# Kernel optimization log

Hardware: AMD Instinct MI355X
Metric: run time of the kernel (lower is better)

Reference implementation:

```python
import jax, jax.numpy as jnp
import numpy as np

K_SIZE, STRIDE, PAD = 3, 1, 1
B, C1, C2, H, W = 2, 256, 256, 64, 64


def conv2d(x, w, b, stride, pad):
    out = jax.lax.conv_general_dilated(
        x, w, (stride, stride), [(pad, pad), (pad, pad)],
        dimension_numbers=("NCHW", "OIHW", "NCHW"))
    return out + b[None, :, None, None]


def deform_conv2d(x, offset, mask, w, b, k, stride, pad):
    # torchvision.ops.deform_conv2d semantics (modulated, offset_groups=1)
    Bn, C, Hh, Ww = x.shape
    Ho, Wo = offset.shape[2], offset.shape[3]
    K = k * k
    # offset channels are (dy, dx) interleaved per kernel point
    off = offset.reshape(Bn, K, 2, Ho, Wo)
    dy, dx = off[:, :, 0], off[:, :, 1]          # [B,K,Ho,Wo]
    ki = jnp.arange(k)
    kyy, kxx = jnp.meshgrid(ki, ki, indexing="ij")
    kyy, kxx = kyy.reshape(K), kxx.reshape(K)
    base_y = (jnp.arange(Ho) * stride - pad)[None, :, None] + kyy[:, None, None]  # [K,Ho,1]
    base_x = (jnp.arange(Wo) * stride - pad)[None, None, :] + kxx[:, None, None]  # [K,1,Wo]
    ys = base_y[None].astype(x.dtype) + dy       # [B,K,Ho,Wo]
    xs = base_x[None].astype(x.dtype) + dx
    N = K * Ho * Wo
    ysf, xsf = ys.reshape(Bn, N), xs.reshape(Bn, N)
    y0 = jnp.floor(ysf)
    x0 = jnp.floor(xsf)
    ly, lx = ysf - y0, xsf - x0                  # bilinear fractions
    y0i, x0i = y0.astype(jnp.int32), x0.astype(jnp.int32)
    xf = x.reshape(Bn, C, Hh * Ww)

    def gather(yi, xi):
        valid = (yi >= 0) & (yi < Hh) & (xi >= 0) & (xi < Ww)
        idx = jnp.clip(yi, 0, Hh - 1) * Ww + jnp.clip(xi, 0, Ww - 1)
        v = jnp.take_along_axis(xf, idx[:, None, :], axis=2)  # [B,C,N]
        return v * valid[:, None, :].astype(x.dtype)

    v00 = gather(y0i, x0i)
    v01 = gather(y0i, x0i + 1)
    v10 = gather(y0i + 1, x0i)
    v11 = gather(y0i + 1, x0i + 1)
    wy1, wx1 = ly[:, None], lx[:, None]
    val = (v00 * (1 - wy1) * (1 - wx1) + v01 * (1 - wy1) * wx1 +
           v10 * wy1 * (1 - wx1) + v11 * wy1 * wx1)          # [B,C,N]
    val = val.reshape(Bn, C, K, Ho, Wo) * mask[:, None]       # modulate
    out = jnp.einsum("ock,bckhw->bohw", w.reshape(w.shape[0], C, K), val)
    return out + b[None, :, None, None]


def setup_inputs() -> dict:
    key = jax.random.key(0)
    ks = jax.random.split(key, 6)
    k2 = K_SIZE * K_SIZE
    return {
        "x": jax.random.normal(ks[0], (B, C1, H, W), jnp.float32),
        "offset_feat": jax.random.normal(ks[1], (B, C2, H, W), jnp.float32),
        # offset/mask head conv (zero-init in module; small random so offsets are non-trivial)
        "w_offset_mask": jax.random.normal(ks[2], (3 * k2, C2, K_SIZE, K_SIZE), jnp.float32) * 0.01,
        "b_offset_mask": jax.random.normal(ks[3], (3 * k2,), jnp.float32) * 0.01,
        "w_dcn": jax.random.normal(ks[4], (C2, C1, K_SIZE, K_SIZE), jnp.float32) / np.sqrt(C1 * k2),
        "b_dcn": jax.random.normal(ks[5], (C2,), jnp.float32) * 0.01,
    }


def reference(x, offset_feat, w_offset_mask, b_offset_mask, w_dcn, b_dcn):
    om = conv2d(offset_feat, w_offset_mask, b_offset_mask, STRIDE, PAD)  # [B,3*k*k,Ho,Wo]
    o1, o2, m = jnp.split(om, 3, axis=1)
    offset = jnp.concatenate([o1, o2], axis=1)   # [B,2*k*k,Ho,Wo]
    mask = jax.nn.sigmoid(m)                      # [B,k*k,Ho,Wo]
    return deform_conv2d(x, offset, mask, w_dcn, b_dcn, K_SIZE, STRIDE, PAD)
```

## Files before the change

### kernel.cpp

```cpp
#include <hip/hip_runtime.h>
#include <math.h>

#define BATCH 2
#define CIN   256
#define COUT  256
#define HWPIX 4096
#define CKTOT 2304
#define VSTR  40
#define PH    66
#define PHW   4356
#define VBUF  (288 * VSTR)

typedef __attribute__((ext_vector_type(8))) short short8;
typedef __attribute__((ext_vector_type(2))) float float2v;
typedef __attribute__((ext_vector_type(4))) float float4v;

__device__ __forceinline__ unsigned short f2bf(float f) {
    unsigned u = __float_as_uint(f);
    unsigned r = (u + 0x7FFFu + ((u >> 16) & 1u)) >> 16;
    return (unsigned short)r;
}
__device__ __forceinline__ float bf2f(unsigned short h) {
    return __uint_as_float(((unsigned)h) << 16);
}
__device__ __forceinline__ unsigned cvtpk_bf16(float a, float b) {
    unsigned r;
    asm("v_cvt_pk_bf16_f32 %0, %1, %2" : "=v"(r) : "v"(a), "v"(b));
    return r;
}
__device__ __forceinline__ float2v unpk(unsigned u) {
    float2v r;
    r.x = __uint_as_float(u << 16);
    r.y = __uint_as_float(u & 0xffff0000u);
    return r;
}

__global__ __launch_bounds__(256) void prep_kernel(
    const float* __restrict__ x, const float* __restrict__ feat,
    const float* __restrict__ wdcn, const float* __restrict__ wom,
    unsigned short* __restrict__ xTh,
    unsigned short* __restrict__ fh,
    unsigned short* __restrict__ whi,
    unsigned short* __restrict__ wohi)
{
    const int bid = blockIdx.x;
    const int tid = threadIdx.x;

    if (bid < 4096) {
        const bool isx = bid < 2048;
        const int lb = isx ? bid : bid - 2048;
        const int b  = lb >> 10;
        const int r  = lb & 1023;
        const int pt = r >> 3;
        const int ct = r & 7;
        __shared__ float t[32][33];
        const int tx = tid & 31, ty = tid >> 5;
        const float* src = isx ? x : feat;
        const float* sb = src + ((size_t)b * 256 + ct * 32) * HWPIX + pt * 32;
#pragma unroll
        for (int i = ty; i < 32; i += 8)
            t[i][tx] = sb[(size_t)i * HWPIX + tx];
        __syncthreads();
        const int px = tid >> 3;
        const int c4 = (tid & 7) << 2;
        float a0 = t[c4][px], a1 = t[c4 + 1][px];
        float a2 = t[c4 + 2][px], a3 = t[c4 + 3][px];
        uint2 rv = make_uint2(cvtpk_bf16(a0, a1), cvtpk_bf16(a2, a3));
        if (isx) {
            *(uint2*)&xTh[((size_t)b * HWPIX + pt * 32 + px) * 256 + ct * 32 + c4] = rv;
        } else {
            int p = pt * 32 + px;
            int row = (p >> 6) + 1, col = (p & 63) + 1;
            *(uint2*)&fh[((size_t)b * PHW + row * PH + col) * 256 + ct * 32 + c4] = rv;
        }
    } else if (bid < 5248) {
        int g2 = (bid - 4096) * 256 + tid;
        int e  = g2 * 2;
        int cc  = e & 31;
        int co  = (e >> 5) & 255;
        int kcb = e >> 13;
        int k   = kcb >> 3;
        int cb  = kcb & 7;
        const float* s = wdcn + ((size_t)co * 256 + cb * 32 + cc) * 9 + k;
        *(unsigned*)&whi[e] = cvtpk_bf16(s[0], s[9]);
    } else if (bid < 5536) {
        int gid = (bid - 5248) * 256 + tid;
        int cc  = gid & 31;
        int co  = (gid >> 5) & 31;
        int kcb = gid >> 10;
        int k   = kcb >> 3;
        int cb  = kcb & 7;
        float w = 0.0f;
        if (co < 27) w = wom[(size_t)co * CKTOT + (cb * 32 + cc) * 9 + k];
        wohi[gid] = f2bf(w);
    } else {
        int idx = (bid - 5536) * 256 + tid;
        int b = idx / 66560;
        int r = idx - b * 66560;
        int pidx = r >> 8;
        int c = r & 255;
        int row, col;
        if (pidx < 66)       { row = 0;           col = pidx; }
        else if (pidx < 132) { row = 65;          col = pidx - 66; }
        else if (pidx < 196) { row = pidx - 131;  col = 0; }
        else                 { row = pidx - 195;  col = 65; }
        fh[((size_t)b * PHW + row * PH + col) * 256 + c] = 0;
    }
}

__global__ __launch_bounds__(512, 2) void dcn_fused_kernel(
    const unsigned short* __restrict__ xTh,
    const unsigned short* __restrict__ fh,
    const unsigned short* __restrict__ whi,
    const unsigned short* __restrict__ wohi,
    const float* __restrict__ bom,
    const float* __restrict__ bdcn,
    float* __restrict__ out)
{
    const int tid = threadIdx.x;
    const int y   = blockIdx.x >> 1;
    const int xh  = blockIdx.x & 1;
    const int b   = blockIdx.y;

    __shared__ __align__(16) char smem[2 * VBUF * 2 + 288 * 16 + 288 * 16];
    float (*red)[32][32]   = (float (*)[32][32])smem;
    unsigned short* V      = (unsigned short*)smem;
    float4* s_wt           = (float4*)(smem + 2 * VBUF * 2);
    int4*   s_ix           = (int4*)(smem + 2 * VBUF * 2 + 288 * 16);

    const int wv   = tid >> 6;
    const int lane = tid & 63;
    const int l15  = lane & 15;
    const int q    = lane >> 4;

    {
        float4v aco[2][2];
#pragma unroll
        for (int t = 0; t < 2; ++t)
#pragma unroll
            for (int p = 0; p < 2; ++p) aco[t][p] = (float4v)0.0f;

        const unsigned short* fhb = fh + (size_t)b * PHW * 256;
#pragma unroll 3
        for (int i = 0; i < 9; ++i) {
            int kcb = wv * 9 + i;
            int k  = kcb >> 3;
            int cb = kcb & 7;
            size_t s = ((size_t)((y + k / 3) * PH + xh * 32 + (k % 3))) * 256
                     + cb * 32 + q * 8;
            short8 bh0 = *(const short8*)(fhb + s + (size_t)l15 * 256);
            short8 bh1 = *(const short8*)(fhb + s + (size_t)(16 + l15) * 256);
            short8 ah0 = *(const short8*)(wohi + ((size_t)kcb * 32 + l15) * 32 + q * 8);
            short8 ah1 = *(const short8*)(wohi + ((size_t)kcb * 32 + 16 + l15) * 32 + q * 8);
            aco[0][0] = __builtin_amdgcn_mfma_f32_16x16x32_bf16(ah0, bh0, aco[0][0], 0, 0, 0);
            aco[0][1] = __builtin_amdgcn_mfma_f32_16x16x32_bf16(ah0, bh1, aco[0][1], 0, 0, 0);
            aco[1][0] = __builtin_amdgcn_mfma_f32_16x16x32_bf16(ah1, bh0, aco[1][0], 0, 0, 0);
            aco[1][1] = __builtin_amdgcn_mfma_f32_16x16x32_bf16(ah1, bh1, aco[1][1], 0, 0, 0);
        }
#pragma unroll
        for (int t = 0; t < 2; ++t)
#pragma unroll
            for (int p = 0; p < 2; ++p)
#pragma unroll
                for (int r = 0; r < 4; ++r)
                    red[wv][t * 16 + q * 4 + r][p * 16 + l15] = aco[t][p][r];
    }
    __syncthreads();

    if (tid < 288) {
        int k   = tid >> 5;
        int pxl = tid & 31;
        float dy = bom[2 * k], dx = bom[2 * k + 1], mm = bom[18 + k];
#pragma unroll
        for (int g = 0; g < 8; ++g) {
            dy += red[g][2 * k][pxl];
            dx += red[g][2 * k + 1][pxl];
            mm += red[g][18 + k][pxl];
        }
        int xx = xh * 32 + pxl;
        float ys = (float)(y  - 1 + (k / 3)) + dy;
        float xs = (float)(xx - 1 + (k % 3)) + dx;
        float y0f = floorf(ys), x0f = floorf(xs);
        int y0 = (int)y0f, x0 = (int)x0f;
        float ly = ys - y0f, lx = xs - x0f;
        float m  = 1.0f / (1.0f + expf(-mm));
        bool yv0 = ((unsigned)y0 < 64u), yv1 = ((unsigned)(y0 + 1) < 64u);
        bool xv0 = ((unsigned)x0 < 64u), xv1 = ((unsigned)(x0 + 1) < 64u);
        int i00 = (y0 * 64 + x0) << 8;
        float4 wt;
        int4 ix;
        wt.x = (yv0 && xv0) ? (1.0f - ly) * (1.0f - lx) * m : 0.0f;
        wt.y = (yv0 && xv1) ? (1.0f - ly) * lx * m          : 0.0f;
        wt.z = (yv1 && xv0) ? ly * (1.0f - lx) * m          : 0.0f;
        wt.w = (yv1 && xv1) ? ly * lx * m                   : 0.0f;
        ix.x = (yv0 && xv0) ? i00          : 0;
        ix.y = (yv0 && xv1) ? i00 + 256    : 0;
        ix.z = (yv1 && xv0) ? i00 + 16384  : 0;
        ix.w = (yv1 && xv1) ? i00 + 16640  : 0;
        s_wt[tid] = wt;
        s_ix[tid] = ix;
    }
    __syncthreads();

    const int w = tid >> 6;

    const int cg   = tid & 3;
    const int spx  = (tid >> 2) & 31;
    const int tapg = tid >> 7;

    int4   rix[3];
    float4 rwt[3];
#pragma unroll
    for (int j = 0; j < 3; ++j) {
        int k = tapg + 4 * j;
        if (k > 8) continue;
        rix[j] = s_ix[k * 32 + spx];
        rwt[j] = s_wt[k * 32 + spx];
    }

    float4v acc[2][2];
#pragma unroll
    for (int t = 0; t < 2; ++t)
#pragma unroll
        for (int p = 0; p < 2; ++p) acc[t][p] = (float4v)0.0f;

    const unsigned short* xc0 = xTh + ((size_t)b << 12) * 256 + cg * 8;

    uint4 pf[3][4];

    auto gload = [&](int cb) {
        const unsigned short* xc = xc0 + cb * 32;
#pragma unroll
        for (int j = 0; j < 3; ++j) {
            int k = tapg + 4 * j;
            if (k > 8) continue;
            int4 ix = rix[j];
            pf[j][0] = *(const uint4*)(xc + ix.x);
            pf[j][1] = *(const uint4*)(xc + ix.y);
            pf[j][2] = *(const uint4*)(xc + ix.z);
            pf[j][3] = *(const uint4*)(xc + ix.w);
        }
    };
    auto interp = [&](int buf) {
#pragma unroll
        for (int j = 0; j < 3; ++j) {
            int k = tapg + 4 * j;
            if (k > 8) continue;
            int cidx = k * 32 + spx;
            float4 wt = rwt[j];
            const unsigned* u00 = (const unsigned*)&pf[j][0];
            const unsigned* u01 = (const unsigned*)&pf[j][1];
            const unsigned* u10 = (const unsigned*)&pf[j][2];
            const unsigned* u11 = (const unsigned*)&pf[j][3];
            unsigned hv[4];
#pragma unroll
            for (int jj = 0; jj < 4; ++jj) {
                float2v s = unpk(u00[jj]) * wt.x;
                s += unpk(u01[jj]) * wt.y;
                s += unpk(u10[jj]) * wt.z;
                s += unpk(u11[jj]) * wt.w;
                hv[jj] = cvtpk_bf16(s.x, s.y);
            }
            *(uint4*)&V[buf * VBUF + cidx * VSTR + cg * 8]
                = make_uint4(hv[0], hv[1], hv[2], hv[3]);
        }
    };

    gload(0);

    for (int cb = 0; cb < 8; ++cb) {
        const int buf = cb & 1;
        interp(buf);
        if (cb < 7) gload(cb + 1);
        __syncthreads();

#pragma unroll 3
        for (int k = 0; k < 9; ++k) {
            const int kcb = k * 8 + cb;
            size_t base = ((size_t)kcb * 256 + w * 32 + l15) * 32 + q * 8;
            short8 ah0 = *(const short8*)(whi + base);
            short8 ah1 = *(const short8*)(whi + base + 16 * 32);
            short8 bh0 = *(const short8*)&V[buf * VBUF + (k * 32 + l15) * VSTR + q * 8];
            short8 bh1 = *(const short8*)&V[buf * VBUF + (k * 32 + 16 + l15) * VSTR + q * 8];
            acc[0][0] = __builtin_amdgcn_mfma_f32_16x16x32_bf16(ah0, bh0, acc[0][0], 0, 0, 0);
            acc[0][1] = __builtin_amdgcn_mfma_f32_16x16x32_bf16(ah0, bh1, acc[0][1], 0, 0, 0);
            acc[1][0] = __builtin_amdgcn_mfma_f32_16x16x32_bf16(ah1, bh0, acc[1][0], 0, 0, 0);
            acc[1][1] = __builtin_amdgcn_mfma_f32_16x16x32_bf16(ah1, bh1, acc[1][1], 0, 0, 0);
        }
    }

#pragma unroll
    for (int t = 0; t < 2; ++t) {
#pragma unroll
        for (int r = 0; r < 4; ++r) {
            int co = w * 32 + t * 16 + q * 4 + r;
            float bias = bdcn[co];
#pragma unroll
            for (int p = 0; p < 2; ++p) {
                int px = xh * 32 + p * 16 + l15;
                out[(((size_t)b * COUT + co) << 12) + y * 64 + px]
                    = acc[t][p][r] + bias;
            }
        }
    }
}

extern "C" void kernel_launch(void* const* d_in, const int* in_sizes, int n_in,
                              void* d_out, int out_size, void* d_ws, size_t ws_size,
                              hipStream_t stream)
{
    const float* x    = (const float*)d_in[0];
    const float* feat = (const float*)d_in[1];
    const float* wom  = (const float*)d_in[2];
    const float* bom  = (const float*)d_in[3];
    const float* wdcn = (const float*)d_in[4];
    const float* bdcn = (const float*)d_in[5];
    float* out = (float*)d_out;

    unsigned short* whi  = (unsigned short*)d_ws;
    unsigned short* wohi = whi + (size_t)CKTOT * 256;
    unsigned short* xTh  = wohi + 73728;
    unsigned short* fh   = xTh + (size_t)2 * HWPIX * 256;

    prep_kernel<<<6056, 256, 0, stream>>>(x, feat, wdcn, wom, xTh, fh,
                                          whi, wohi);

    dim3 grid(128, 2);
    dcn_fused_kernel<<<grid, 512, 0, stream>>>(xTh, fh, whi, wohi,
                                               bom, bdcn, out);
}
```

Baseline: 120.1 us.

## Split output channels across two blocks to double grid and raise occupancy

Adds a grid dimension that splits the 256 output channels into two halves. Each block now computes 128 output channels with half the accumulators, so the grid doubles to 512 blocks and launch bounds allow 4 blocks per CU. In exchange, both halves redo the offset/mask conv and the bilinear sampling of the input, doubling that redundant gather and interpolation work. Sampling indices and weights are read from shared memory each time instead of being cached in registers.

```diff
diff --git a/kernel.cpp b/kernel.cpp
--- a/kernel.cpp
+++ b/kernel.cpp
@@ -1,9 +1,6 @@
 #include <hip/hip_runtime.h>
 #include <math.h>
 
-#define BATCH 2
-#define CIN   256
-#define COUT  256
 #define HWPIX 4096
 #define CKTOT 2304
 #define VSTR  40
@@ -108,7 +105,7 @@
     }
 }
 
-__global__ __launch_bounds__(512, 2) void dcn_fused_kernel(
+__global__ __launch_bounds__(512, 4) void dcn_fused_kernel(
     const unsigned short* __restrict__ xTh,
     const unsigned short* __restrict__ fh,
     const unsigned short* __restrict__ whi,
@@ -120,7 +117,8 @@
     const int tid = threadIdx.x;
     const int y   = blockIdx.x >> 1;
     const int xh  = blockIdx.x & 1;
-    const int b   = blockIdx.y;
+    const int cog = blockIdx.y;
+    const int b   = blockIdx.z;
 
     __shared__ __align__(16) char smem[2 * VBUF * 2 + 288 * 16 + 288 * 16];
     float (*red)[32][32]   = (float (*)[32][32])smem;
@@ -204,27 +202,15 @@
 
     const int w = tid >> 6;
 
-    const int cg   = tid & 3;
+    const int cg2  = tid & 3;
     const int spx  = (tid >> 2) & 31;
     const int tapg = tid >> 7;
 
-    int4   rix[3];
-    float4 rwt[3];
-#pragma unroll
-    for (int j = 0; j < 3; ++j) {
-        int k = tapg + 4 * j;
-        if (k > 8) continue;
-        rix[j] = s_ix[k * 32 + spx];
-        rwt[j] = s_wt[k * 32 + spx];
-    }
-
-    float4v acc[2][2];
-#pragma unroll
-    for (int t = 0; t < 2; ++t)
-#pragma unroll
-        for (int p = 0; p < 2; ++p) acc[t][p] = (float4v)0.0f;
-
-    const unsigned short* xc0 = xTh + ((size_t)b << 12) * 256 + cg * 8;
+    float4v acc[2];
+    acc[0] = (float4v)0.0f;
+    acc[1] = (float4v)0.0f;
+
+    const unsigned short* xc0 = xTh + ((size_t)b << 12) * 256 + cg2 * 8;
 
     uint4 pf[3][4];
 
@@ -234,7 +220,7 @@
         for (int j = 0; j < 3; ++j) {
             int k = tapg + 4 * j;
             if (k > 8) continue;
-            int4 ix = rix[j];
+            int4 ix = s_ix[k * 32 + spx];
             pf[j][0] = *(const uint4*)(xc + ix.x);
             pf[j][1] = *(const uint4*)(xc + ix.y);
             pf[j][2] = *(const uint4*)(xc + ix.z);
@@ -247,7 +233,7 @@
             int k = tapg + 4 * j;
             if (k > 8) continue;
             int cidx = k * 32 + spx;
-            float4 wt = rwt[j];
+            float4 wt = s_wt[cidx];
             const unsigned* u00 = (const unsigned*)&pf[j][0];
             const unsigned* u01 = (const unsigned*)&pf[j][1];
             const unsigned* u10 = (const unsigned*)&pf[j][2];
@@ -261,7 +247,7 @@
                 s += unpk(u11[jj]) * wt.w;
                 hv[jj] = cvtpk_bf16(s.x, s.y);
             }
-            *(uint4*)&V[buf * VBUF + cidx * VSTR + cg * 8]
+            *(uint4*)&V[buf * VBUF + cidx * VSTR + cg2 * 8]
                 = make_uint4(hv[0], hv[1], hv[2], hv[3]);
         }
     };
@@ -277,30 +263,24 @@
 #pragma unroll 3
         for (int k = 0; k < 9; ++k) {
             const int kcb = k * 8 + cb;
-            size_t base = ((size_t)kcb * 256 + w * 32 + l15) * 32 + q * 8;
-            short8 ah0 = *(const short8*)(whi + base);
-            short8 ah1 = *(const short8*)(whi + base + 16 * 32);
+            size_t base = ((size_t)kcb * 256 + cog * 128 + w * 16 + l15) * 32 + q * 8;
+            short8 ah  = *(const short8*)(whi + base);
             short8 bh0 = *(const short8*)&V[buf * VBUF + (k * 32 + l15) * VSTR + q * 8];
             short8 bh1 = *(const short8*)&V[buf * VBUF + (k * 32 + 16 + l15) * VSTR + q * 8];
-            acc[0][0] = __builtin_amdgcn_mfma_f32_16x16x32_bf16(ah0, bh0, acc[0][0], 0, 0, 0);
-            acc[0][1] = __builtin_amdgcn_mfma_f32_16x16x32_bf16(ah0, bh1, acc[0][1], 0, 0, 0);
-            acc[1][0] = __builtin_amdgcn_mfma_f32_16x16x32_bf16(ah1, bh0, acc[1][0], 0, 0, 0);
-            acc[1][1] = __builtin_amdgcn_mfma_f32_16x16x32_bf16(ah1, bh1, acc[1][1], 0, 0, 0);
-        }
-    }
-
-#pragma unroll
-    for (int t = 0; t < 2; ++t) {
-#pragma unroll
-        for (int r = 0; r < 4; ++r) {
-            int co = w * 32 + t * 16 + q * 4 + r;
-            float bias = bdcn[co];
-#pragma unroll
-            for (int p = 0; p < 2; ++p) {
-                int px = xh * 32 + p * 16 + l15;
-                out[(((size_t)b * COUT + co) << 12) + y * 64 + px]
-                    = acc[t][p][r] + bias;
-            }
+            acc[0] = __builtin_amdgcn_mfma_f32_16x16x32_bf16(ah, bh0, acc[0], 0, 0, 0);
+            acc[1] = __builtin_amdgcn_mfma_f32_16x16x32_bf16(ah, bh1, acc[1], 0, 0, 0);
+        }
+    }
+
+#pragma unroll
+    for (int r = 0; r < 4; ++r) {
+        int co = cog * 128 + w * 16 + q * 4 + r;
+        float bias = bdcn[co];
+#pragma unroll
+        for (int p = 0; p < 2; ++p) {
+            int px = xh * 32 + p * 16 + l15;
+            out[(((size_t)b * 256 + co) << 12) + y * 64 + px]
+                = acc[p][r] + bias;
         }
     }
 }
@@ -325,7 +305,7 @@
     prep_kernel<<<6056, 256, 0, stream>>>(x, feat, wdcn, wom, xTh, fh,
                                           whi, wohi);
 
-    dim3 grid(128, 2);
+    dim3 grid(128, 2, 2);
     dcn_fused_kernel<<<grid, 512, 0, stream>>>(xTh, fh, whi, wohi,
                                                bom, bdcn, out);
 }
```

New measurement: 121.5 us. Within noise of the previous version (+1.2%).
